# Performance work log

Measured on AMD Instinct MI355X. Metric: run time of the kernel, lower is better.

## Reference

```python
import jax, jax.numpy as jnp
import numpy as np
from jax import lax

STRIDE = 16
OFFSET = 8.0  # vgg16 backbone
C = 512
A = 9  # 3 ratios x 3 scales
THR = 0.05
IOU_THR = 0.7
N_OUT = 50
K = 2048  # fixed candidate budget for jit-able NMS

# anchors: rows of [[1,1],[1,2],[2,1]] * scale for scale in (128,256,512) -> [9,2] (w,h)
ANCHORS = np.concatenate([np.array([[1, 1], [1, 2], [2, 1]], np.float32) * s
                          for s in (128.0, 256.0, 512.0)], axis=0)


def _conv(x, w, b, pad):
    y = lax.conv_general_dilated(x, w, (1, 1), [(pad, pad), (pad, pad)],
                                 dimension_numbers=("NCHW", "OIHW", "NCHW"))
    return y + b[None, :, None, None]


def setup_inputs() -> dict:
    key = jax.random.key(0)
    ks = jax.random.split(key, 8)
    x = jax.random.normal(ks[0], (4, C, 64, 96), dtype=jnp.float32)
    w1 = jax.random.normal(ks[1], (C, C, 3, 3), dtype=jnp.float32) * 0.02
    b1 = jnp.zeros((C,), jnp.float32)
    w_cls = jax.random.normal(ks[2], (2 * A, C, 1, 1), dtype=jnp.float32) * 0.02
    b_cls = jnp.zeros((2 * A,), jnp.float32)
    w_reg = jax.random.normal(ks[3], (4 * A, C, 1, 1), dtype=jnp.float32) * 0.02
    b_reg = jnp.zeros((4 * A,), jnp.float32)
    return {"x": x, "w1": w1, "b1": b1, "w_cls": w_cls, "b_cls": b_cls,
            "w_reg": w_reg, "b_reg": b_reg, "h": 1024, "w": 1536}


def _rpn_forward(x, w1, b1, w_cls, b_cls, w_reg, b_reg, h, w):
    B = x.shape[0]
    f = _conv(x, w1, b1, 1)                      # [B,512,H,W] (no activation in original)
    cls = _conv(f, w_cls, b_cls, 0)              # [B,2A,H,W]
    cls = jax.nn.softmax(cls, axis=1)            # Softmax2d: over ALL 2A channels
    reg = _conv(f, w_reg, b_reg, 0)              # [B,4A,H,W]
    H, W = cls.shape[-2:]
    prob_fg = cls.reshape(B, A, 2, H, W)[:, :, 1]           # [B,A,H,W]
    reg = reg.reshape(B, A, 4, H, W).transpose(0, 1, 3, 4, 2)  # [B,A,H,W,4]

    scores = prob_fg.reshape(-1)                  # [B*A*H*W]
    reg_flat = reg.reshape(-1, 4)

    # threshold (torch.where) -> fixed-size top-K preselection for jit
    masked = jnp.where(scores >= THR, scores, -1.0)
    top_s, top_i = lax.top_k(masked, K)          # sorted descending
    valid = top_s >= THR

    # recover (a, y, x) from flat index; batch index is dropped (as in original NMS)
    aidx = (top_i // (H * W)) % A
    yidx = (top_i // W) % H
    xidx = top_i % W

    off_x = (w - OFFSET * 2) % STRIDE / 2 + OFFSET
    off_y = (h - OFFSET * 2) % STRIDE / 2 + OFFSET
    cx = xidx.astype(jnp.float32) * STRIDE + off_x
    cy = yidx.astype(jnp.float32) * STRIDE + off_y
    anc = jnp.asarray(ANCHORS)[aidx]             # [K,2] (w,h)

    r = reg_flat[top_i]                          # [K,4]
    bx = r[:, 0] * anc[:, 0] + cx
    by = r[:, 1] * anc[:, 1] + cy
    bw = jnp.exp(r[:, 2]) * anc[:, 0]
    bh = jnp.exp(r[:, 3]) * anc[:, 1]
    x1 = bx - bw * 0.5
    y1 = by - bh * 0.5
    x2 = bx + bw * 0.5
    y2 = by + bh * 0.5
    boxes = jnp.stack([x1, y1, x2, y2], axis=1)  # [K,4] xyxy

    # pairwise IoU [K,K]
    area = (x2 - x1) * (y2 - y1)
    ix1 = jnp.maximum(x1[:, None], x1[None, :])
    iy1 = jnp.maximum(y1[:, None], y1[None, :])
    ix2 = jnp.minimum(x2[:, None], x2[None, :])
    iy2 = jnp.minimum(y2[:, None], y2[None, :])
    inter = jnp.clip(ix2 - ix1, 0.0) * jnp.clip(iy2 - iy1, 0.0)
    iou = inter / (area[:, None] + area[None, :] - inter + 1e-9)

    idx = jnp.arange(K)

    def body(i, keep):
        sup = keep[i] & (iou[i] > IOU_THR) & (idx > i)
        return keep & ~sup

    keep = lax.fori_loop(0, K, body, valid)

    final_s = jnp.where(keep, top_s, -1.0)
    sel_s, sel_i = lax.top_k(final_s, N_OUT)     # first N kept, score order
    out_valid = sel_s >= THR
    out_scores = jnp.where(out_valid, sel_s, 0.0)
    out_boxes = jnp.where(out_valid[:, None], boxes[sel_i], 0.0)
    return out_scores, out_boxes


def reference(x, w1, b1, w_cls, b_cls, w_reg, b_reg, h, w):
    return _rpn_forward(x, w1, b1, w_cls, b_cls, w_reg, b_reg, h, w)
```

## Files before the change

kernel.cpp:

```cpp
#include <hip/hip_runtime.h>
#include <stdint.h>

#define NB 4
#define NC 512
#define NH 64
#define NW 96
#define NA 9
#define NPIX (NB*NA*NH*NW)
#define KSEL 2048
#define NOUT 50
#define THRS 0.05f

#define HIST_BASE 0x3D4CCu
#define HIST_SIZE 9024
#define CAND_CAP 8192

typedef _Float16 half8 __attribute__((ext_vector_type(8)));
typedef float floatx16 __attribute__((ext_vector_type(16)));

__device__ const float ANC_W[9] = {128.f,128.f,256.f,256.f,256.f,512.f,512.f,512.f,1024.f};
__device__ const float ANC_H[9] = {128.f,256.f,128.f,256.f,512.f,256.f,512.f,1024.f,512.f};

__global__ __launch_bounds__(256) void wexp2_k(const float* __restrict__ w1,
                                               uint4* __restrict__ wexp2) {
    __shared__ __align__(16) _Float16 lbuf[36 * 32 * 8];
    const int bid = blockIdx.x;
    const int cc = bid >> 4, cog = bid & 15;
    const int t = threadIdx.x;
    const int co_l = t >> 3, j = t & 7;
    const int co = cog * 32 + co_l;
    const float* r0 = w1 + ((size_t)co * 512 + cc * 16 + j) * 9;
    const float* r1 = r0 + 8 * 9;
#pragma unroll
    for (int kk = 0; kk < 9; ++kk) {
        const float v0 = r0[kk] * 1024.f;
        const float v1 = r1[kk] * 1024.f;
        const _Float16 h0 = (_Float16)v0, h1 = (_Float16)v1;
        const _Float16 l0 = (_Float16)(v0 - (float)h0);
        const _Float16 l1 = (_Float16)(v1 - (float)h1);
        lbuf[((kk * 4 + 0) * 32 + co_l) * 8 + j] = h0;
        lbuf[((kk * 4 + 1) * 32 + co_l) * 8 + j] = h1;
        lbuf[((kk * 4 + 2) * 32 + co_l) * 8 + j] = l0;
        lbuf[((kk * 4 + 3) * 32 + co_l) * 8 + j] = l1;
    }
    __syncthreads();
    for (int e = t; e < 1152; e += 256) {
        const int co_e = e & 31;
        const int rest = e >> 5;
        const int kk = rest >> 2, kd = rest & 3;
        const uint4 v = *(const uint4*)&lbuf[(rest * 32 + co_e) * 8];
        wexp2[(((size_t)(cc * 9 + kk) * 4 + kd) * 512) + cog * 32 + co_e] = v;
    }
}

#define XS_BYTES 20800
#define WB_BYTES 16384
#define CONV_LDS (XS_BYTES + 2*WB_BYTES)

__global__ __launch_bounds__(512, 2) void conv_mfma(
    const float* __restrict__ x, const uint4* __restrict__ wexp2,
    const float* __restrict__ b1, float* __restrict__ f)
{
    __shared__ __align__(16) char smem[CONV_LDS];
    char* xs = smem;
    char* wb = smem + XS_BYTES;
    const int t = threadIdx.x;
    const int bid = blockIdx.x;
    const int half = bid & 1, pxb = bid >> 1;
    const int b = pxb >> 5, r = pxb & 31, by = r >> 2, bx = r & 3;
    const int y0 = by * 8, x0 = bx * 24;
    const int wq = t >> 6, lane = t & 63;
    const int hpx = wq >> 2, qc = wq & 3;
    const int m32 = lane & 31, khalf = lane >> 5;

    int abase[3];
#pragma unroll
    for (int mt = 0; mt < 3; ++mt) {
        const int px = hpx * 96 + mt * 32 + m32;
        const int yl = px / 24, xl = px - yl * 24;
        abase[mt] = (yl * 26 + xl) * 80 + khalf * 16;
    }
    const int bbase = khalf * 4096 + (qc * 64 + m32) * 16;

    floatx16 acc[3][2];
#pragma unroll
    for (int mt = 0; mt < 3; ++mt)
#pragma unroll
        for (int nt = 0; nt < 2; ++nt)
#pragma unroll
            for (int i = 0; i < 16; ++i) acc[mt][nt][i] = 0.f;

    const int co_l = t & 255, pp = t >> 8;
    const uint4* wsrc = wexp2 + half * 256 + co_l;
    uint4 pf0, pf1;
    auto loadw = [&](int q2) {
        const size_t base = (size_t)q2 * 2048;
        pf0 = wsrc[base + (size_t)pp * 512];
        pf1 = wsrc[base + (size_t)(pp + 2) * 512];
    };
    const int wa0 = pp * 4096 + co_l * 16;
    const int wa1 = (pp + 2) * 4096 + co_l * 16;

    const float* xb = x + (size_t)b * NC * (NH * NW);

    loadw(0);
    *(uint4*)(wb + wa0) = pf0;
    *(uint4*)(wb + wa1) = pf1;
    loadw(1);

    int cc = 0, kk = 0;
    for (int q = 0; q < 288; ++q) {
        if (kk == 0) {
            __syncthreads();
            const float* xc = xb + (size_t)cc * 16 * (NH * NW);
            for (int it = t; it < 520; it += 512) {
                const int kh = (it >= 260) ? 1 : 0;
                const int slot = it - kh * 260;
                const int ya = slot / 26, xa = slot - ya * 26;
                const int gy = y0 - 1 + ya, gx = x0 - 1 + xa;
                const bool ok = (gy >= 0 && gy < NH && gx >= 0 && gx < NW);
                const int off = ok ? (kh * 8 * 6144 + gy * 96 + gx) : 0;
                union { _Float16 h[8]; uint4 u; } hi, lo;
#pragma unroll
                for (int j = 0; j < 8; ++j) {
                    const float v = (ok ? xc[off + j * 6144] : 0.f) * 1024.f;
                    const _Float16 hh = (_Float16)v;
                    hi.h[j] = hh;
                    lo.h[j] = (_Float16)(v - (float)hh);
                }
                *(uint4*)(xs + slot * 80 + kh * 16) = hi.u;
                *(uint4*)(xs + slot * 80 + 32 + kh * 16) = lo.u;
            }
        }
        __syncthreads();
        if (q < 287) {
            char* wd = wb + ((q + 1) & 1) * WB_BYTES;
            *(uint4*)(wd + wa0) = pf0;
            *(uint4*)(wd + wa1) = pf1;
            if (q < 286) loadw(q + 2);
        }
        {
            const int ky = kk / 3, kx = kk - ky * 3;
            const char* xcur = xs + (ky * 26 + kx) * 80;
            half8 axh[3], axl[3];
#pragma unroll
            for (int mt = 0; mt < 3; ++mt) {
                axh[mt] = *(const half8*)(xcur + abase[mt]);
                axl[mt] = *(const half8*)(xcur + abase[mt] + 32);
            }
            const char* wc = wb + (q & 1) * WB_BYTES + bbase;
            half8 bwh[2], bwl[2];
#pragma unroll
            for (int nt = 0; nt < 2; ++nt) {
                bwh[nt] = *(const half8*)(wc + nt * 512);
                bwl[nt] = *(const half8*)(wc + 8192 + nt * 512);
            }
#pragma unroll
            for (int nt = 0; nt < 2; ++nt)
#pragma unroll
                for (int mt = 0; mt < 3; ++mt)
                    acc[mt][nt] = __builtin_amdgcn_mfma_f32_32x32x16_f16(
                        axh[mt], bwh[nt], acc[mt][nt], 0, 0, 0);
#pragma unroll
            for (int nt = 0; nt < 2; ++nt)
#pragma unroll
                for (int mt = 0; mt < 3; ++mt)
                    acc[mt][nt] = __builtin_amdgcn_mfma_f32_32x32x16_f16(
                        axh[mt], bwl[nt], acc[mt][nt], 0, 0, 0);
#pragma unroll
            for (int nt = 0; nt < 2; ++nt)
#pragma unroll
                for (int mt = 0; mt < 3; ++mt)
                    acc[mt][nt] = __builtin_amdgcn_mfma_f32_32x32x16_f16(
                        axl[mt], bwh[nt], acc[mt][nt], 0, 0, 0);
        }
        if (++kk == 9) { kk = 0; ++cc; }
    }

    const float inv = 1.0f / 1048576.0f;
#pragma unroll
    for (int mt = 0; mt < 3; ++mt)
#pragma unroll
        for (int nt = 0; nt < 2; ++nt) {
            const int co = half * 256 + qc * 64 + nt * 32 + m32;
            const float bias = b1[co];
#pragma unroll
            for (int reg = 0; reg < 16; ++reg) {
                const int row = (reg & 3) + 8 * (reg >> 2) + 4 * khalf;
                const int pxl = hpx * 96 + mt * 32 + row;
                const int yl = pxl / 24, xl = pxl - yl * 24;
                const size_t gpx = (size_t)(b * 64 + y0 + yl) * 96 + (x0 + xl);
                f[gpx * 512 + co] = acc[mt][nt][reg] * inv + bias;
            }
        }
}

__global__ __launch_bounds__(256) void head_k(
    const float* __restrict__ f, const float* __restrict__ wcls,
    const float* __restrict__ wreg, float* __restrict__ part)
{
    __shared__ __align__(16) float smem[14336];
    float* ftile = smem;
    float* wls = smem + 256 * 36;
    const int t = threadIdx.x;
    const int px0 = blockIdx.x * 256;
    const int qd = blockIdx.y;
    float acc[54];
#pragma unroll
    for (int oc = 0; oc < 54; ++oc) acc[oc] = 0.f;

    for (int sub = 0; sub < 4; ++sub) {
        const int ci0 = qd * 128 + sub * 32;
        __syncthreads();
        for (int e = t; e < 8192; e += 256) {
            const int p = e >> 5, c = e & 31;
            ftile[p * 36 + c] = f[(size_t)(px0 + p) * 512 + ci0 + c];
        }
        for (int e = t; e < 1728; e += 256) {
            const int oc = e >> 5, c = e & 31;
            wls[oc * 32 + c] = (oc < 18) ? wcls[oc * 512 + ci0 + c]
                                         : wreg[(oc - 18) * 512 + ci0 + c];
        }
        __syncthreads();
        float fr[32];
#pragma unroll
        for (int c4 = 0; c4 < 8; ++c4) {
            const float4 v = *(const float4*)&ftile[t * 36 + c4 * 4];
            fr[c4 * 4 + 0] = v.x; fr[c4 * 4 + 1] = v.y;
            fr[c4 * 4 + 2] = v.z; fr[c4 * 4 + 3] = v.w;
        }
#pragma unroll
        for (int oc = 0; oc < 54; ++oc) {
            const float4* wrow = (const float4*)&wls[oc * 32];
            float s = 0.f;
#pragma unroll
            for (int c4 = 0; c4 < 8; ++c4) {
                const float4 wv = wrow[c4];
                s += fr[c4 * 4 + 0] * wv.x + fr[c4 * 4 + 1] * wv.y +
                     fr[c4 * 4 + 2] * wv.z + fr[c4 * 4 + 3] * wv.w;
            }
            acc[oc] += s;
        }
    }
    __syncthreads();
    float* otile = smem;
#pragma unroll
    for (int oc = 0; oc < 54; ++oc) otile[t * 56 + oc] = acc[oc];
    __syncthreads();
    for (int e = t; e < 14336; e += 256) {
        const int oc = e >> 8, p = e & 255;
        part[(size_t)(qd * 56 + oc) * 24576 + px0 + p] = otile[p * 56 + oc];
    }
}

__global__ __launch_bounds__(256) void combine_k(
    const float* __restrict__ part, const float* __restrict__ bcls,
    const float* __restrict__ breg, float* __restrict__ scores,
    float* __restrict__ regs)
{
    const int px = blockIdx.x * 256 + threadIdx.x;
    float lg[54];
#pragma unroll
    for (int oc = 0; oc < 54; ++oc) {
        float s = 0.f;
#pragma unroll
        for (int qd = 0; qd < 4; ++qd)
            s += part[(size_t)(qd * 56 + oc) * 24576 + px];
        lg[oc] = s;
    }
    float cl[18];
    float m = -1e30f;
#pragma unroll
    for (int oc = 0; oc < 18; ++oc) {
        cl[oc] = lg[oc] + bcls[oc];
        m = fmaxf(m, cl[oc]);
    }
    float sum = 0.f;
#pragma unroll
    for (int oc = 0; oc < 18; ++oc) { cl[oc] = expf(cl[oc] - m); sum += cl[oc]; }
    const float inv = 1.f / sum;
    const int b = px / 6144;
    const int yx = px - b * 6144;
#pragma unroll
    for (int a = 0; a < 9; ++a) {
        const int idx = b * 55296 + a * 6144 + yx;
        scores[idx] = cl[2 * a + 1] * inv;
        float4 rv;
        rv.x = lg[18 + a * 4 + 0] + breg[a * 4 + 0];
        rv.y = lg[18 + a * 4 + 1] + breg[a * 4 + 1];
        rv.z = lg[18 + a * 4 + 2] + breg[a * 4 + 2];
        rv.w = lg[18 + a * 4 + 3] + breg[a * 4 + 3];
        ((float4*)regs)[idx] = rv;
    }
}

__global__ void hist_k(const float* __restrict__ scores, uint32_t* __restrict__ hist) {
    const int i = blockIdx.x * 256 + threadIdx.x;
    const float s = scores[i];
    if (s >= THRS) {
        int bkt = (int)(__float_as_uint(s) >> 12) - (int)HIST_BASE;
        bkt = min(max(bkt, 0), HIST_SIZE - 1);
        atomicAdd(&hist[bkt], 1u);
    }
}

__global__ void scan_k(const uint32_t* __restrict__ hist, uint32_t* __restrict__ ctl) {
    __shared__ uint32_t ssum[1024];
    const int t = threadIdx.x;
    uint32_t s = 0;
#pragma unroll
    for (int u = 0; u < 9; ++u) {
        const int bkt = t * 9 + u;
        if (bkt < HIST_SIZE) s += hist[bkt];
    }
    const uint32_t mysum = s;
    ssum[t] = s;
    __syncthreads();
    for (int off = 1; off < 1024; off <<= 1) {
        uint32_t v = (t + off < 1024) ? ssum[t + off] : 0u;
        __syncthreads();
        ssum[t] += v;
        __syncthreads();
    }
    const uint32_t total = ssum[0];
    const uint32_t above = (t < 1023) ? ssum[t + 1] : 0u;
    if (total < KSEL) {
        if (t == 0) ctl[0] = HIST_BASE;
    } else if (above < KSEL && above + mysum >= KSEL) {
        uint32_t run = above;
        for (int u = 8; u >= 0; --u) {
            const int bkt = t * 9 + u;
            if (bkt >= HIST_SIZE) continue;
            run += hist[bkt];
            if (run >= KSEL) { ctl[0] = HIST_BASE + (uint32_t)bkt; break; }
        }
    }
}

__global__ void collect_k(const float* __restrict__ scores, uint32_t* __restrict__ ctl,
                          uint64_t* __restrict__ cand) {
    const int i = blockIdx.x * 256 + threadIdx.x;
    const float s = scores[i];
    if (s >= THRS) {
        const uint32_t bits = __float_as_uint(s);
        if ((bits >> 12) >= ctl[0]) {
            const uint32_t pos = atomicAdd(&ctl[1], 1u);
            if (pos < CAND_CAP)
                cand[pos] = ((uint64_t)bits << 32) | (uint64_t)(0xFFFFFFFFu - (uint32_t)i);
        }
    }
}

__global__ void sort_decode_k(const uint64_t* __restrict__ cand, const uint32_t* __restrict__ ctl,
                              const float* __restrict__ regs,
                              const int* __restrict__ hp, const int* __restrict__ wp,
                              float* __restrict__ tops_s, float* __restrict__ boxes) {
    __shared__ uint64_t keys[CAND_CAP];
    const int t = threadIdx.x;
    const int M = min((int)ctl[1], CAND_CAP);
    const int N = (M <= 4096) ? 4096 : 8192;
    for (int k = t; k < N; k += 1024) keys[k] = (k < M) ? cand[k] : 0ull;
    __syncthreads();
    for (int size = 2; size <= N; size <<= 1) {
        for (int stride = size >> 1; stride > 0; stride >>= 1) {
            for (int k = t; k < N; k += 1024) {
                const int p = k ^ stride;
                if (p > k) {
                    const uint64_t a = keys[k], bb = keys[p];
                    const bool sw = ((k & size) == 0) ? (a < bb) : (a > bb);
                    if (sw) { keys[k] = bb; keys[p] = a; }
                }
            }
            __syncthreads();
        }
    }
    const int w_in = wp[0], h_in = hp[0];
    const float offx = (float)((w_in - 16) % 16) * 0.5f + 8.0f;
    const float offy = (float)((h_in - 16) % 16) * 0.5f + 8.0f;
    for (int k = t; k < KSEL; k += 1024) {
        const uint64_t key = keys[k];
        float sc = -1.f, x1 = 0.f, y1 = 0.f, x2 = 0.f, y2 = 0.f;
        if (k < M && key != 0ull) {
            const uint32_t idx = 0xFFFFFFFFu - (uint32_t)(key & 0xFFFFFFFFull);
            sc = __uint_as_float((uint32_t)(key >> 32));
            const int a  = (int)(idx / (NH * NW)) % NA;
            const int yy = (int)(idx / NW) % NH;
            const int xx = (int)(idx % NW);
            const float4 r = ((const float4*)regs)[idx];
            const float aw = ANC_W[a], ah = ANC_H[a];
            const float cx = (float)xx * 16.f + offx;
            const float cy = (float)yy * 16.f + offy;
            const float bx = r.x * aw + cx;
            const float by = r.y * ah + cy;
            const float bw = expf(r.z) * aw;
            const float bh = expf(r.w) * ah;
            x1 = bx - bw * 0.5f; y1 = by - bh * 0.5f;
            x2 = bx + bw * 0.5f; y2 = by + bh * 0.5f;
        }
        tops_s[k] = sc;
        ((float4*)boxes)[k] = make_float4(x1, y1, x2, y2);
    }
}

__global__ void iou_k(const float* __restrict__ boxes, uint64_t* __restrict__ mask) {
    __shared__ float4 jb[64];
    const int t = threadIdx.x;
    const int bi = blockIdx.x, bj = blockIdx.y;
    jb[t] = ((const float4*)boxes)[bj * 64 + t];
    __syncthreads();
    const int i = bi * 64 + t;
    const float4 mb = ((const float4*)boxes)[i];
    const float areai = (mb.z - mb.x) * (mb.w - mb.y);
    uint64_t w = 0;
    for (int jj = 0; jj < 64; ++jj) {
        const float4 ob = jb[jj];
        const int j = bj * 64 + jj;
        const float ix1 = fmaxf(mb.x, ob.x);
        const float iy1 = fmaxf(mb.y, ob.y);
        const float ix2 = fminf(mb.z, ob.z);
        const float iy2 = fminf(mb.w, ob.w);
        const float inter = fmaxf(ix2 - ix1, 0.f) * fmaxf(iy2 - iy1, 0.f);
        const float areaj = (ob.z - ob.x) * (ob.w - ob.y);
        const float iou = inter / (areai + areaj - inter + 1e-9f);
        if (iou > 0.7f && j > i) w |= (1ull << jj);
    }
    mask[(size_t)i * 32 + bj] = w;
}

__global__ void nms_k(const float* __restrict__ tops_s, const float* __restrict__ boxes,
                      const uint64_t* __restrict__ mask, float* __restrict__ out) {
    __shared__ uint64_t remv[32];
    __shared__ float ssc[KSEL];
    __shared__ int sel[NOUT];
    const int t = threadIdx.x;
    for (int k = t; k < KSEL; k += 64) ssc[k] = tops_s[k];
    if (t < 32) remv[t] = 0ull;
    uint64_t nextrow = (t < 32) ? mask[t] : 0ull;
    int cnt = 0;
    for (int i = 0; i < KSEL && cnt < NOUT; ++i) {
        const uint64_t cur = nextrow;
        if (t < 32 && i + 1 < KSEL) nextrow = mask[(size_t)(i + 1) * 32 + t];
        const uint64_t rw = remv[i >> 6];
        const bool sup = (rw >> (i & 63)) & 1ull;
        if (ssc[i] >= THRS && !sup) {
            if (t < 32) remv[t] |= cur;
            if (t == 0) sel[cnt] = i;
            ++cnt;
        }
    }
    for (int k = t; k < NOUT; k += 64) {
        float s = 0.f;
        float4 bb = make_float4(0.f, 0.f, 0.f, 0.f);
        if (k < cnt) { const int i = sel[k]; s = ssc[i]; bb = ((const float4*)boxes)[i]; }
        out[k] = s;
        out[NOUT + k * 4 + 0] = bb.x;
        out[NOUT + k * 4 + 1] = bb.y;
        out[NOUT + k * 4 + 2] = bb.z;
        out[NOUT + k * 4 + 3] = bb.w;
    }
}

extern "C" void kernel_launch(void* const* d_in, const int* in_sizes, int n_in,
                              void* d_out, int out_size, void* d_ws, size_t ws_size,
                              hipStream_t stream) {
    const float* x    = (const float*)d_in[0];
    const float* w1   = (const float*)d_in[1];
    const float* b1   = (const float*)d_in[2];
    const float* wcls = (const float*)d_in[3];
    const float* bcls = (const float*)d_in[4];
    const float* wreg = (const float*)d_in[5];
    const float* breg = (const float*)d_in[6];
    const int*   hp   = (const int*)d_in[7];
    const int*   wp   = (const int*)d_in[8];
    float* out = (float*)d_out;

    char* ws = (char*)d_ws;
    size_t off = 0;
    auto carve = [&](size_t bytes) -> void* {
        void* p = ws + off;
        off = (off + bytes + 255) & ~(size_t)255;
        return p;
    };
    uint4*    wexp2  = (uint4*)carve((size_t)288 * 4 * 512 * 16);
    float*    f      = (float*)carve((size_t)24576 * 512 * 4);
    float*    part   = (float*)carve((size_t)4 * 56 * 24576 * 4);
    float*    scores = (float*)carve((size_t)NPIX * 4);
    float*    regs   = (float*)carve((size_t)NPIX * 16);
    uint32_t* hist   = (uint32_t*)carve((size_t)HIST_SIZE * 4);
    uint32_t* ctl    = (uint32_t*)carve(256);
    uint64_t* cand   = (uint64_t*)carve((size_t)CAND_CAP * 8);
    float*    tops_s = (float*)carve((size_t)KSEL * 4);
    float*    boxes  = (float*)carve((size_t)KSEL * 16);
    uint64_t* mask   = (uint64_t*)carve((size_t)KSEL * 32 * 8);
    (void)ws_size; (void)in_sizes; (void)n_in; (void)out_size;

    hipMemsetAsync(hist, 0, (size_t)HIST_SIZE * 4, stream);
    hipMemsetAsync(ctl, 0, 256, stream);

    wexp2_k<<<512, 256, 0, stream>>>(w1, wexp2);
    conv_mfma<<<256, 512, 0, stream>>>(x, wexp2, b1, f);
    head_k<<<dim3(96, 4), 256, 0, stream>>>(f, wcls, wreg, part);
    combine_k<<<96, 256, 0, stream>>>(part, bcls, breg, scores, regs);
    hist_k<<<NPIX / 256, 256, 0, stream>>>(scores, hist);
    scan_k<<<1, 1024, 0, stream>>>(hist, ctl);
    collect_k<<<NPIX / 256, 256, 0, stream>>>(scores, ctl, cand);
    sort_decode_k<<<1, 1024, 0, stream>>>(cand, ctl, regs, hp, wp, tops_s, boxes);
    iou_k<<<dim3(KSEL / 64, KSEL / 64), 64, 0, stream>>>(boxes, mask);
    nms_k<<<1, 64, 0, stream>>>(tops_s, boxes, mask, out);
}
```

Measured before the change: 684.3 us.

## Split conv into quarter-channel blocks with 3-tap weight groups and fuse head with combine

The conv kernel now runs 512 blocks of 256 threads, each covering 128 output channels instead of 256. Each barrier-separated step loads weights for three kernel taps at once, which cuts the barrier count per block from about 288 to 96 but drops double buffering of the weight tile. The 1x1 head kernel now accumulates over all 512 input channels in one block of 128 pixels and applies softmax and bias directly. This removes the partial-sum buffer and the separate combine kernel. The tradeoffs are that the input tile is restaged twice as many times overall, and each head thread reads its f row directly from global memory with long strides.

```diff
diff --git a/kernel.cpp b/kernel.cpp
--- a/kernel.cpp
+++ b/kernel.cpp
@@ -54,10 +54,10 @@
 }
 
 #define XS_BYTES 20800
-#define WB_BYTES 16384
-#define CONV_LDS (XS_BYTES + 2*WB_BYTES)
-
-__global__ __launch_bounds__(512, 2) void conv_mfma(
+#define WB_BYTES 24576
+#define CONV_LDS (XS_BYTES + WB_BYTES)
+
+__global__ __launch_bounds__(256, 2) void conv_mfma(
     const float* __restrict__ x, const uint4* __restrict__ wexp2,
     const float* __restrict__ b1, float* __restrict__ f)
 {
@@ -66,11 +66,11 @@
     char* wb = smem + XS_BYTES;
     const int t = threadIdx.x;
     const int bid = blockIdx.x;
-    const int half = bid & 1, pxb = bid >> 1;
+    const int qco = bid & 3, pxb = bid >> 2;
     const int b = pxb >> 5, r = pxb & 31, by = r >> 2, bx = r & 3;
     const int y0 = by * 8, x0 = bx * 24;
-    const int wq = t >> 6, lane = t & 63;
-    const int hpx = wq >> 2, qc = wq & 3;
+    const int wv = t >> 6, lane = t & 63;
+    const int hpx = wv >> 1, nh = wv & 1;
     const int m32 = lane & 31, khalf = lane >> 5;
 
     int abase[3];
@@ -80,7 +80,7 @@
         const int yl = px / 24, xl = px - yl * 24;
         abase[mt] = (yl * 26 + xl) * 80 + khalf * 16;
     }
-    const int bbase = khalf * 4096 + (qc * 64 + m32) * 16;
+    const int bb0 = khalf * 2048 + (nh * 64 + m32) * 16;
 
     floatx16 acc[3][2];
 #pragma unroll
@@ -90,70 +90,72 @@
 #pragma unroll
             for (int i = 0; i < 16; ++i) acc[mt][nt][i] = 0.f;
 
-    const int co_l = t & 255, pp = t >> 8;
-    const uint4* wsrc = wexp2 + half * 256 + co_l;
-    uint4 pf0, pf1;
-    auto loadw = [&](int q2) {
-        const size_t base = (size_t)q2 * 2048;
-        pf0 = wsrc[base + (size_t)pp * 512];
-        pf1 = wsrc[base + (size_t)(pp + 2) * 512];
+    const int co_l = t & 127, pp = t >> 7;
+    const uint4* wsrc = wexp2 + qco * 128 + co_l;
+    uint4 pf[3][2];
+    auto loadw3 = [&](int g2) {
+#pragma unroll
+        for (int c3 = 0; c3 < 3; ++c3) {
+            const size_t base = (size_t)(3 * g2 + c3) * 2048;
+            pf[c3][0] = wsrc[base + (size_t)pp * 512];
+            pf[c3][1] = wsrc[base + (size_t)(pp + 2) * 512];
+        }
     };
-    const int wa0 = pp * 4096 + co_l * 16;
-    const int wa1 = (pp + 2) * 4096 + co_l * 16;
+    const int wa0 = pp * 2048 + co_l * 16;
+    const int wa1 = (pp + 2) * 2048 + co_l * 16;
 
     const float* xb = x + (size_t)b * NC * (NH * NW);
-
-    loadw(0);
-    *(uint4*)(wb + wa0) = pf0;
-    *(uint4*)(wb + wa1) = pf1;
-    loadw(1);
-
-    int cc = 0, kk = 0;
-    for (int q = 0; q < 288; ++q) {
-        if (kk == 0) {
-            __syncthreads();
-            const float* xc = xb + (size_t)cc * 16 * (NH * NW);
-            for (int it = t; it < 520; it += 512) {
-                const int kh = (it >= 260) ? 1 : 0;
-                const int slot = it - kh * 260;
-                const int ya = slot / 26, xa = slot - ya * 26;
-                const int gy = y0 - 1 + ya, gx = x0 - 1 + xa;
-                const bool ok = (gy >= 0 && gy < NH && gx >= 0 && gx < NW);
-                const int off = ok ? (kh * 8 * 6144 + gy * 96 + gx) : 0;
-                union { _Float16 h[8]; uint4 u; } hi, lo;
-#pragma unroll
-                for (int j = 0; j < 8; ++j) {
-                    const float v = (ok ? xc[off + j * 6144] : 0.f) * 1024.f;
-                    const _Float16 hh = (_Float16)v;
-                    hi.h[j] = hh;
-                    lo.h[j] = (_Float16)(v - (float)hh);
-                }
-                *(uint4*)(xs + slot * 80 + kh * 16) = hi.u;
-                *(uint4*)(xs + slot * 80 + 32 + kh * 16) = lo.u;
-            }
-        }
-        __syncthreads();
-        if (q < 287) {
-            char* wd = wb + ((q + 1) & 1) * WB_BYTES;
-            *(uint4*)(wd + wa0) = pf0;
-            *(uint4*)(wd + wa1) = pf1;
-            if (q < 286) loadw(q + 2);
-        }
-        {
-            const int ky = kk / 3, kx = kk - ky * 3;
-            const char* xcur = xs + (ky * 26 + kx) * 80;
+    auto stage_x = [&](int cc) {
+        const float* xc = xb + (size_t)cc * 16 * (NH * NW);
+        for (int it = t; it < 520; it += 256) {
+            const int kh = (it >= 260) ? 1 : 0;
+            const int slot = it - kh * 260;
+            const int ya = slot / 26, xa = slot - ya * 26;
+            const int gy = y0 - 1 + ya, gx = x0 - 1 + xa;
+            const bool ok = (gy >= 0 && gy < NH && gx >= 0 && gx < NW);
+            const int off = ok ? (kh * 8 * 6144 + gy * 96 + gx) : 0;
+            union { _Float16 h[8]; uint4 u; } hi, lo;
+#pragma unroll
+            for (int j = 0; j < 8; ++j) {
+                const float v = (ok ? xc[off + j * 6144] : 0.f) * 1024.f;
+                const _Float16 hh = (_Float16)v;
+                hi.h[j] = hh;
+                lo.h[j] = (_Float16)(v - (float)hh);
+            }
+            *(uint4*)(xs + slot * 80 + kh * 16) = hi.u;
+            *(uint4*)(xs + slot * 80 + 32 + kh * 16) = lo.u;
+        }
+    };
+
+    loadw3(0);
+    stage_x(0);
+
+    for (int g = 0; g < 96; ++g) {
+        const int ky = g % 3, cc = g / 3;
+        __syncthreads();
+#pragma unroll
+        for (int c3 = 0; c3 < 3; ++c3) {
+            *(uint4*)(wb + c3 * 8192 + wa0) = pf[c3][0];
+            *(uint4*)(wb + c3 * 8192 + wa1) = pf[c3][1];
+        }
+        if (ky == 0 && g > 0) stage_x(cc);
+        __syncthreads();
+        if (g < 95) loadw3(g + 1);
+#pragma unroll
+        for (int c3 = 0; c3 < 3; ++c3) {
+            const char* xcur = xs + (ky * 26 + c3) * 80;
             half8 axh[3], axl[3];
 #pragma unroll
             for (int mt = 0; mt < 3; ++mt) {
                 axh[mt] = *(const half8*)(xcur + abase[mt]);
                 axl[mt] = *(const half8*)(xcur + abase[mt] + 32);
             }
-            const char* wc = wb + (q & 1) * WB_BYTES + bbase;
+            const char* wc = wb + c3 * 8192 + bb0;
             half8 bwh[2], bwl[2];
 #pragma unroll
             for (int nt = 0; nt < 2; ++nt) {
                 bwh[nt] = *(const half8*)(wc + nt * 512);
-                bwl[nt] = *(const half8*)(wc + 8192 + nt * 512);
+                bwl[nt] = *(const half8*)(wc + 4096 + nt * 512);
             }
 #pragma unroll
             for (int nt = 0; nt < 2; ++nt)
@@ -174,7 +176,6 @@
                     acc[mt][nt] = __builtin_amdgcn_mfma_f32_32x32x16_f16(
                         axl[mt], bwh[nt], acc[mt][nt], 0, 0, 0);
         }
-        if (++kk == 9) { kk = 0; ++cc; }
     }
 
     const float inv = 1.0f / 1048576.0f;
@@ -182,7 +183,7 @@
     for (int mt = 0; mt < 3; ++mt)
 #pragma unroll
         for (int nt = 0; nt < 2; ++nt) {
-            const int co = half * 256 + qc * 64 + nt * 32 + m32;
+            const int co = qco * 128 + nh * 64 + nt * 32 + m32;
             const float bias = b1[co];
 #pragma unroll
             for (int reg = 0; reg < 16; ++reg) {
@@ -197,100 +198,72 @@
 
 __global__ __launch_bounds__(256) void head_k(
     const float* __restrict__ f, const float* __restrict__ wcls,
-    const float* __restrict__ wreg, float* __restrict__ part)
-{
-    __shared__ __align__(16) float smem[14336];
-    float* ftile = smem;
-    float* wls = smem + 256 * 36;
-    const int t = threadIdx.x;
-    const int px0 = blockIdx.x * 256;
-    const int qd = blockIdx.y;
-    float acc[54];
-#pragma unroll
-    for (int oc = 0; oc < 54; ++oc) acc[oc] = 0.f;
-
-    for (int sub = 0; sub < 4; ++sub) {
-        const int ci0 = qd * 128 + sub * 32;
-        __syncthreads();
-        for (int e = t; e < 8192; e += 256) {
-            const int p = e >> 5, c = e & 31;
-            ftile[p * 36 + c] = f[(size_t)(px0 + p) * 512 + ci0 + c];
-        }
-        for (int e = t; e < 1728; e += 256) {
-            const int oc = e >> 5, c = e & 31;
-            wls[oc * 32 + c] = (oc < 18) ? wcls[oc * 512 + ci0 + c]
-                                         : wreg[(oc - 18) * 512 + ci0 + c];
-        }
-        __syncthreads();
-        float fr[32];
-#pragma unroll
-        for (int c4 = 0; c4 < 8; ++c4) {
-            const float4 v = *(const float4*)&ftile[t * 36 + c4 * 4];
-            fr[c4 * 4 + 0] = v.x; fr[c4 * 4 + 1] = v.y;
-            fr[c4 * 4 + 2] = v.z; fr[c4 * 4 + 3] = v.w;
-        }
-#pragma unroll
-        for (int oc = 0; oc < 54; ++oc) {
-            const float4* wrow = (const float4*)&wls[oc * 32];
-            float s = 0.f;
-#pragma unroll
-            for (int c4 = 0; c4 < 8; ++c4) {
-                const float4 wv = wrow[c4];
-                s += fr[c4 * 4 + 0] * wv.x + fr[c4 * 4 + 1] * wv.y +
-                     fr[c4 * 4 + 2] * wv.z + fr[c4 * 4 + 3] * wv.w;
-            }
-            acc[oc] += s;
-        }
-    }
-    __syncthreads();
-    float* otile = smem;
-#pragma unroll
-    for (int oc = 0; oc < 54; ++oc) otile[t * 56 + oc] = acc[oc];
-    __syncthreads();
-    for (int e = t; e < 14336; e += 256) {
-        const int oc = e >> 8, p = e & 255;
-        part[(size_t)(qd * 56 + oc) * 24576 + px0 + p] = otile[p * 56 + oc];
-    }
-}
-
-__global__ __launch_bounds__(256) void combine_k(
-    const float* __restrict__ part, const float* __restrict__ bcls,
+    const float* __restrict__ wreg, const float* __restrict__ bcls,
     const float* __restrict__ breg, float* __restrict__ scores,
     float* __restrict__ regs)
 {
-    const int px = blockIdx.x * 256 + threadIdx.x;
-    float lg[54];
-#pragma unroll
-    for (int oc = 0; oc < 54; ++oc) {
-        float s = 0.f;
-#pragma unroll
-        for (int qd = 0; qd < 4; ++qd)
-            s += part[(size_t)(qd * 56 + oc) * 24576 + px];
-        lg[oc] = s;
-    }
-    float cl[18];
-    float m = -1e30f;
-#pragma unroll
-    for (int oc = 0; oc < 18; ++oc) {
-        cl[oc] = lg[oc] + bcls[oc];
-        m = fmaxf(m, cl[oc]);
-    }
-    float sum = 0.f;
-#pragma unroll
-    for (int oc = 0; oc < 18; ++oc) { cl[oc] = expf(cl[oc] - m); sum += cl[oc]; }
-    const float inv = 1.f / sum;
-    const int b = px / 6144;
-    const int yx = px - b * 6144;
-#pragma unroll
-    for (int a = 0; a < 9; ++a) {
-        const int idx = b * 55296 + a * 6144 + yx;
-        scores[idx] = cl[2 * a + 1] * inv;
-        float4 rv;
-        rv.x = lg[18 + a * 4 + 0] + breg[a * 4 + 0];
-        rv.y = lg[18 + a * 4 + 1] + breg[a * 4 + 1];
-        rv.z = lg[18 + a * 4 + 2] + breg[a * 4 + 2];
-        rv.w = lg[18 + a * 4 + 3] + breg[a * 4 + 3];
-        ((float4*)regs)[idx] = rv;
+    __shared__ __align__(16) float smem[6912 + 128 * 57];
+    float* wls = smem;
+    float* lt  = smem + 6912;
+    const int t = threadIdx.x;
+    const int px0 = blockIdx.x * 128;
+    const int px_l = t & 127, oh = t >> 7;
+    float acc27[27];
+#pragma unroll
+    for (int k = 0; k < 27; ++k) acc27[k] = 0.f;
+
+    for (int qd = 0; qd < 4; ++qd) {
+        __syncthreads();
+        for (int e = t; e < 6912; e += 256) {
+            const int oc = e >> 7, c = e & 127;
+            wls[e] = (oc < 18) ? wcls[oc * 512 + qd * 128 + c]
+                               : wreg[(oc - 18) * 512 + qd * 128 + c];
+        }
+        __syncthreads();
+        const float4* fp = (const float4*)(f + (size_t)(px0 + px_l) * 512 + qd * 128);
+        const float4* wp4 = (const float4*)wls;
+#pragma unroll 4
+        for (int c4 = 0; c4 < 32; ++c4) {
+            const float4 fv = fp[c4];
+#pragma unroll
+            for (int k = 0; k < 27; ++k) {
+                const float4 wv = wp4[(oh * 27 + k) * 32 + c4];
+                acc27[k] += fv.x * wv.x + fv.y * wv.y + fv.z * wv.z + fv.w * wv.w;
+            }
+        }
+    }
+    __syncthreads();
+#pragma unroll
+    for (int k = 0; k < 27; ++k) lt[px_l * 57 + oh * 27 + k] = acc27[k];
+    __syncthreads();
+
+    if (t < 128) {
+        const int px = px0 + t;
+        const float* row = lt + t * 57;
+        float cl[18];
+        float m = -1e30f;
+#pragma unroll
+        for (int oc = 0; oc < 18; ++oc) {
+            cl[oc] = row[oc] + bcls[oc];
+            m = fmaxf(m, cl[oc]);
+        }
+        float sum = 0.f;
+#pragma unroll
+        for (int oc = 0; oc < 18; ++oc) { cl[oc] = expf(cl[oc] - m); sum += cl[oc]; }
+        const float inv = 1.f / sum;
+        const int b = px / 6144;
+        const int yx = px - b * 6144;
+#pragma unroll
+        for (int a = 0; a < 9; ++a) {
+            const int idx = b * 55296 + a * 6144 + yx;
+            scores[idx] = cl[2 * a + 1] * inv;
+            float4 rv;
+            rv.x = row[18 + a * 4 + 0] + breg[a * 4 + 0];
+            rv.y = row[18 + a * 4 + 1] + breg[a * 4 + 1];
+            rv.z = row[18 + a * 4 + 2] + breg[a * 4 + 2];
+            rv.w = row[18 + a * 4 + 3] + breg[a * 4 + 3];
+            ((float4*)regs)[idx] = rv;
+        }
     }
 }
 
@@ -483,7 +456,6 @@
     };
     uint4*    wexp2  = (uint4*)carve((size_t)288 * 4 * 512 * 16);
     float*    f      = (float*)carve((size_t)24576 * 512 * 4);
-    float*    part   = (float*)carve((size_t)4 * 56 * 24576 * 4);
     float*    scores = (float*)carve((size_t)NPIX * 4);
     float*    regs   = (float*)carve((size_t)NPIX * 16);
     uint32_t* hist   = (uint32_t*)carve((size_t)HIST_SIZE * 4);
@@ -498,9 +470,8 @@
     hipMemsetAsync(ctl, 0, 256, stream);
 
     wexp2_k<<<512, 256, 0, stream>>>(w1, wexp2);
-    conv_mfma<<<256, 512, 0, stream>>>(x, wexp2, b1, f);
-    head_k<<<dim3(96, 4), 256, 0, stream>>>(f, wcls, wreg, part);
-    combine_k<<<96, 256, 0, stream>>>(part, bcls, breg, scores, regs);
+    conv_mfma<<<512, 256, 0, stream>>>(x, wexp2, b1, f);
+    head_k<<<192, 256, 0, stream>>>(f, wcls, wreg, bcls, breg, scores, regs);
     hist_k<<<NPIX / 256, 256, 0, stream>>>(scores, hist);
     scan_k<<<1, 1024, 0, stream>>>(hist, ctl);
     collect_k<<<NPIX / 256, 256, 0, stream>>>(scores, ctl, cand);
```

New measurement: 916.3 us. 33.9% more time.
